# Optimization experiments

Measured on AMD Instinct MI355X. Metric: run time of the kernel, lower is better.

## Reference

```python
import jax, jax.numpy as jnp
import numpy as np

B, S, H, NH = 2, 2048, 1024, 16
HD = H // NH  # 64


def setup_inputs() -> dict:
    key = jax.random.key(0)
    ks = jax.random.split(key, 9)
    w = lambda k: jax.random.normal(k, (H, H), dtype=jnp.float32) * 0.02  # torch Linear weight [out,in]
    b = lambda k: jax.random.normal(k, (H,), dtype=jnp.float32) * 0.02
    return {
        "hidden_states": jax.random.normal(ks[0], (B, S, H), dtype=jnp.float32),
        "Wq": w(ks[1]), "bq": b(ks[2]),
        "Wk": w(ks[3]), "bk": b(ks[4]),
        "Wv": w(ks[5]), "bv": b(ks[6]),
        "Wo": w(ks[7]), "bo": b(ks[8]),
    }


def reference(hidden_states, Wq, bq, Wk, bk, Wv, bv, Wo, bo):
    b, s, h = hidden_states.shape
    nh, hd = NH, h // NH

    def proj(W, bias):
        y = hidden_states @ W.T + bias  # torch Linear: x W^T + b
        return y.reshape(b, s, nh, hd).transpose(0, 2, 1, 3)  # [b, h, s, d]

    q = proj(Wq, bq)
    k = proj(Wk, bk)
    v = proj(Wv, bv)

    scale = jnp.sqrt(jnp.asarray(hd, dtype=q.dtype))
    scores = jnp.einsum("bhqd,bhkd->bhqk", q, k) / scale  # [b, h, s, s]
    pos = jnp.arange(s)
    causal = pos[:, None] < pos[None, :]  # True where masked (key after query)
    scores = jnp.where(causal[None, None], -jnp.inf, scores)
    attn = jax.nn.softmax(scores, axis=-1)
    out = jnp.einsum("bhqk,bhkd->bhqd", attn, v)
    out = out.transpose(0, 2, 1, 3).reshape(b, s, h)
    return out @ Wo.T + bo
```

## Files before the change

kernel.cpp:

```cpp
#include <hip/hip_runtime.h>
#include <stdint.h>

typedef __bf16 bf16;
typedef __attribute__((ext_vector_type(2))) __bf16 bf16x2;
typedef __attribute__((ext_vector_type(4))) __bf16 bf16x4;
typedef __attribute__((ext_vector_type(8))) __bf16 bf16x8;
typedef __attribute__((ext_vector_type(4))) float f32x4;
typedef __attribute__((ext_vector_type(4))) short s16x4;

#define B_  2
#define S_  2048
#define H_  1024
#define NH_ 16
#define HD_ 64
#define RS  3072

__device__ __forceinline__ void glds16(const bf16* g, bf16* l) {
  __builtin_amdgcn_global_load_lds(
      (const __attribute__((address_space(1))) uint32_t*)g,
      (__attribute__((address_space(3))) uint32_t*)l, 16, 0, 0);
}

__device__ __forceinline__ f32x4 pv_mfma(bf16x4 a, bf16x4 b, f32x4 c) {
#if __has_builtin(__builtin_amdgcn_mfma_f32_16x16x16bf16_1k)
  union U { bf16x4 h; s16x4 s; };
  U ua; ua.h = a;
  U ub; ub.h = b;
  return __builtin_amdgcn_mfma_f32_16x16x16bf16_1k(ua.s, ub.s, c, 0, 0, 0);
#else
  f32x4 d;
  asm volatile("v_mfma_f32_16x16x16_bf16 %0, %1, %2, %3\n\ts_nop 7\n\ts_nop 7"
               : "=v"(d) : "v"(a), "v"(b), "v"(c));
  return d;
#endif
}

__global__ __launch_bounds__(256) void cvt_f32_bf16(
    const float* __restrict__ s0, bf16* __restrict__ d0, int n0,
    const float* __restrict__ s1, bf16* __restrict__ d1,
    const float* __restrict__ s2, bf16* __restrict__ d2,
    const float* __restrict__ s3, bf16* __restrict__ d3,
    const float* __restrict__ s4, bf16* __restrict__ d4, int nw)
{
  const float* s; bf16* d; int n;
  switch (blockIdx.y) {
    case 0:  s = s0; d = d0; n = n0; break;
    case 1:  s = s1; d = d1; n = nw; break;
    case 2:  s = s2; d = d2; n = nw; break;
    case 3:  s = s3; d = d3; n = nw; break;
    default: s = s4; d = d4; n = nw; break;
  }
  const int i = (blockIdx.x * 256 + threadIdx.x) * 8;
  if (i >= n) return;
  float4 v0 = *(const float4*)(s + i);
  float4 v1 = *(const float4*)(s + i + 4);
  bf16x8 o;
  o[0] = (bf16)v0.x; o[1] = (bf16)v0.y; o[2] = (bf16)v0.z; o[3] = (bf16)v0.w;
  o[4] = (bf16)v1.x; o[5] = (bf16)v1.y; o[6] = (bf16)v1.z; o[7] = (bf16)v1.w;
  *(bf16x8*)(d + i) = o;
}

__global__ __launch_bounds__(512, 2) void gemm_qkv_8ph(
    const bf16* __restrict__ X,
    const bf16* __restrict__ Wc,
    const float* __restrict__ bq, const float* __restrict__ bk,
    const float* __restrict__ bv,
    bf16* __restrict__ Y,
    float qscl)
{
  constexpr int K  = 1024;
  constexpr int NT = K / 64;

  __shared__ __align__(16) bf16 As[2][256 * 64];
  __shared__ __align__(16) bf16 Bs[2][256 * 64];

  const int f   = blockIdx.x;
  const int swz = (f & 7) * 24 + (f >> 3);
  const int by  = swz / 12, bx = swz % 12;
  const int m0  = by * 256, n0 = bx * 256;

  const int tid  = threadIdx.x;
  const int lane = tid & 63;
  const int wave = tid >> 6;
  const int quad = lane >> 4;
  const int l15  = lane & 15;
  const int wm   = (wave >> 2) * 128;
  const int wn   = (wave & 3) * 64;

  const int r0  = tid >> 3;
  const int kc0 = tid & 7;

  const bf16* Xb = X  + (size_t)m0 * K;
  const bf16* Wb = Wc + (size_t)n0 * K;

  f32x4 acc[8][4] = {};

#define SBAR() asm volatile("s_barrier" ::: "memory")
#define VM0()  asm volatile("s_waitcnt vmcnt(0)" ::: "memory")
#define STG(MAT, G, cb_, h)                                                 \
  { _Pragma("unroll") for (int s = 0; s < 2; ++s) {                         \
      const int row = (h) * 128 + s * 64 + r0;                              \
      const int sc  = kc0 ^ (row & 7);                                      \
      glds16((G) + (size_t)row * K + sc * 8,                                \
             &MAT[cb_][((h) * 1024 + s * 512 + wave * 64) * 8]); } }
#define RA(mi, ks) (*(const bf16x8*)&As[cb][(wm + (mi) * 16 + l15) * 64 +   \
                     ((((ks) * 4 + quad)) ^ (l15 & 7)) * 8])
#define RB(ni, ks) (*(const bf16x8*)&Bs[cb][(wn + (ni) * 16 + l15) * 64 +   \
                     ((((ks) * 4 + quad)) ^ (l15 & 7)) * 8])
#define MFMA(d, x, y) d = __builtin_amdgcn_mfma_f32_16x16x32_bf16(x, y, d, 0, 0, 0)

  STG(As, Xb, 0, 0); STG(As, Xb, 0, 1);
  STG(Bs, Wb, 0, 0); STG(Bs, Wb, 0, 1);
  VM0();
  SBAR();

  for (int t = 0; t < NT; ++t) {
    const int cb = t & 1, sb = cb ^ 1;
    const bf16* Xn = Xb + (t + 1) * 64;
    const bf16* Wn = Wb + (t + 1) * 64;
    const bool pre = (t + 1 < NT);

    bf16x8 a[4][2], b[4][2];

#pragma unroll
    for (int mi = 0; mi < 4; ++mi) { a[mi][0] = RA(mi, 0); a[mi][1] = RA(mi, 1); }
#pragma unroll
    for (int ni = 0; ni < 2; ++ni) { b[ni][0] = RB(ni, 0); b[ni][1] = RB(ni, 1); }
    if (pre) { STG(As, Xn, sb, 0); STG(As, Xn, sb, 1); }
    SBAR();
    __builtin_amdgcn_s_setprio(1);
#pragma unroll
    for (int mi = 0; mi < 4; ++mi)
#pragma unroll
      for (int ni = 0; ni < 2; ++ni) {
        MFMA(acc[mi][ni], a[mi][0], b[ni][0]);
        MFMA(acc[mi][ni], a[mi][1], b[ni][1]);
      }
    __builtin_amdgcn_s_setprio(0);
    SBAR();

#pragma unroll
    for (int ni = 2; ni < 4; ++ni) { b[ni][0] = RB(ni, 0); b[ni][1] = RB(ni, 1); }
    if (pre) { STG(Bs, Wn, sb, 0); STG(Bs, Wn, sb, 1); }
    SBAR();
    __builtin_amdgcn_s_setprio(1);
#pragma unroll
    for (int mi = 0; mi < 4; ++mi)
#pragma unroll
      for (int ni = 2; ni < 4; ++ni) {
        MFMA(acc[mi][ni], a[mi][0], b[ni][0]);
        MFMA(acc[mi][ni], a[mi][1], b[ni][1]);
      }
    __builtin_amdgcn_s_setprio(0);
    SBAR();

#pragma unroll
    for (int mi = 0; mi < 4; ++mi) { a[mi][0] = RA(mi + 4, 0); a[mi][1] = RA(mi + 4, 1); }
    SBAR();
    __builtin_amdgcn_s_setprio(1);
#pragma unroll
    for (int mi = 0; mi < 4; ++mi)
#pragma unroll
      for (int ni = 0; ni < 2; ++ni) {
        MFMA(acc[mi + 4][ni], a[mi][0], b[ni][0]);
        MFMA(acc[mi + 4][ni], a[mi][1], b[ni][1]);
      }
    __builtin_amdgcn_s_setprio(0);
    SBAR();

    __builtin_amdgcn_s_setprio(1);
#pragma unroll
    for (int mi = 0; mi < 4; ++mi)
#pragma unroll
      for (int ni = 2; ni < 4; ++ni) {
        MFMA(acc[mi + 4][ni], a[mi][0], b[ni][0]);
        MFMA(acc[mi + 4][ni], a[mi][1], b[ni][1]);
      }
    __builtin_amdgcn_s_setprio(0);
    VM0();
    SBAR();
  }

  const int seg = bx >> 2;
  const float* bias = seg == 0 ? bq : (seg == 1 ? bk : bv);
  const float ysc = seg == 0 ? qscl : 1.0f;
#pragma unroll
  for (int mi = 0; mi < 8; ++mi) {
    const int row = m0 + wm + mi * 16 + quad * 4;
#pragma unroll
    for (int ni = 0; ni < 4; ++ni) {
      const int col = n0 + wn + ni * 16 + l15;
      const float bvv = bias[col & 1023];
#pragma unroll
      for (int r = 0; r < 4; ++r)
        Y[(size_t)(row + r) * RS + col] = (bf16)((acc[mi][ni][r] + bvv) * ysc);
    }
  }
#undef SBAR
#undef VM0
#undef STG
#undef RA
#undef RB
#undef MFMA
}

template <typename TY>
__global__ __launch_bounds__(256) void gemm_bt_bias(
    const bf16* __restrict__ X,
    const bf16* __restrict__ W0, const bf16* __restrict__ W1, const bf16* __restrict__ W2,
    const float* __restrict__ b0, const float* __restrict__ b1, const float* __restrict__ b2,
    TY* __restrict__ Y0, TY* __restrict__ Y1, TY* __restrict__ Y2,
    float ys0, float ys1, float ys2,
    int M, int N, int K)
{
  const bf16* W; const float* bias; TY* Y; float ysc;
  if (blockIdx.z == 0)      { W = W0; bias = b0; Y = Y0; ysc = ys0; }
  else if (blockIdx.z == 1) { W = W1; bias = b1; Y = Y1; ysc = ys1; }
  else                      { W = W2; bias = b2; Y = Y2; ysc = ys2; }

  __shared__ __align__(16) bf16 As[2][128 * 32];
  __shared__ __align__(16) bf16 Bs[2][128 * 32];

  const int tid  = threadIdx.x;
  const int lane = tid & 63;
  const int wave = tid >> 6;
  const int m0 = blockIdx.y * 128;
  const int n0 = blockIdx.x * 128;
  const int wm = (wave >> 1) * 64;
  const int wn = (wave & 1) * 64;

  const int r0 = tid >> 2,            c0 = (tid & 3) * 8;
  const int r1 = (256 + tid) >> 2,    c1 = ((256 + tid) & 3) * 8;
  const int cb0 = (wave * 64) * 8;
  const int cb1 = (256 + wave * 64) * 8;

  f32x4 acc[4][4] = {};

  glds16(X + (size_t)(m0 + r0) * K + c0, &As[0][cb0]);
  glds16(W + (size_t)(n0 + r0) * K + c0, &Bs[0][cb0]);
  glds16(X + (size_t)(m0 + r1) * K + c1, &As[0][cb1]);
  glds16(W + (size_t)(n0 + r1) * K + c1, &Bs[0][cb1]);

  int pb = 0;
  for (int k0 = 0; k0 < K; k0 += 32, pb ^= 1) {
    __syncthreads();

    if (k0 + 32 < K) {
      const int kn = k0 + 32;
      glds16(X + (size_t)(m0 + r0) * K + kn + c0, &As[pb ^ 1][cb0]);
      glds16(W + (size_t)(n0 + r0) * K + kn + c0, &Bs[pb ^ 1][cb0]);
      glds16(X + (size_t)(m0 + r1) * K + kn + c1, &As[pb ^ 1][cb1]);
      glds16(W + (size_t)(n0 + r1) * K + kn + c1, &Bs[pb ^ 1][cb1]);
    }

    bf16x8 a[4], b[4];
#pragma unroll
    for (int i = 0; i < 4; ++i)
      a[i] = *(const bf16x8*)&As[pb][(wm + i * 16 + (lane & 15)) * 32 + (lane >> 4) * 8];
#pragma unroll
    for (int i = 0; i < 4; ++i)
      b[i] = *(const bf16x8*)&Bs[pb][(wn + i * 16 + (lane & 15)) * 32 + (lane >> 4) * 8];
#pragma unroll
    for (int mi = 0; mi < 4; ++mi)
#pragma unroll
      for (int ni = 0; ni < 4; ++ni)
        acc[mi][ni] = __builtin_amdgcn_mfma_f32_16x16x32_bf16(a[mi], b[ni], acc[mi][ni], 0, 0, 0);
  }

#pragma unroll
  for (int mi = 0; mi < 4; ++mi) {
    const int row = m0 + wm + mi * 16 + (lane >> 4) * 4;
#pragma unroll
    for (int ni = 0; ni < 4; ++ni) {
      const int col = n0 + wn + ni * 16 + (lane & 15);
      const float bv = bias[col];
#pragma unroll
      for (int r = 0; r < 4; ++r)
        Y[(size_t)(row + r) * N + col] = (TY)((acc[mi][ni][r] + bv) * ysc);
    }
  }
}

__device__ __forceinline__ void attn_tile_step(
    const bf16* Ksb, const bf16* Vtb, const bf16x8 bq[2], int qrow, int k0,
    bool maskit, float& mr, float& lr, f32x4 oacc[4], int l15, int quad)
{
  f32x4 sacc[8] = {};
  __builtin_amdgcn_s_setprio(1);
#pragma unroll
  for (int ks = 0; ks < 2; ++ks) {
#pragma unroll
    for (int mb = 0; mb < 8; ++mb) {
      const int row = mb * 16 + l15;
      const int ch  = (ks * 4 + quad) ^ (l15 & 7);
      bf16x8 ak = *(const bf16x8*)&Ksb[row * 64 + ch * 8];
      sacc[mb] = __builtin_amdgcn_mfma_f32_16x16x32_bf16(ak, bq[ks], sacc[mb], 0, 0, 0);
    }
  }
  __builtin_amdgcn_s_setprio(0);

  if (maskit) {
#pragma unroll
    for (int mb = 0; mb < 8; ++mb) {
      const int kb = k0 + mb * 16 + quad * 4;
#pragma unroll
      for (int r = 0; r < 4; ++r)
        if (kb + r > qrow) sacc[mb][r] = -1e30f;
    }
  }

  float mx = -1e30f;
#pragma unroll
  for (int mb = 0; mb < 8; ++mb)
    mx = fmaxf(mx, fmaxf(fmaxf(sacc[mb][0], sacc[mb][1]),
                         fmaxf(sacc[mb][2], sacc[mb][3])));
  mx = fmaxf(mx, __shfl_xor(mx, 16, 64));
  mx = fmaxf(mx, __shfl_xor(mx, 32, 64));

  float sum = 0.0f;
  bf16x4 pwv[8];
#pragma unroll
  for (int mb = 0; mb < 8; ++mb) {
    bf16x4 pw;
#pragma unroll
    for (int r = 0; r < 4; ++r) {
      const float p = __builtin_amdgcn_exp2f(sacc[mb][r] - mr);
      sum += p;
      pw[r] = (bf16)p;
    }
    pwv[mb] = pw;
  }
  sum += __shfl_xor(sum, 16, 64);
  sum += __shfl_xor(sum, 32, 64);

  __builtin_amdgcn_s_setprio(1);
#pragma unroll
  for (int mb = 0; mb < 8; ++mb) {
#pragma unroll
    for (int db = 0; db < 4; ++db) {
      const int vch = ((mb * 4 + quad) ^ (l15 & 7)) * 4;
      bf16x4 av = *(const bf16x4*)&Vtb[(db * 16 + l15) * 128 + vch];
      oacc[db] = pv_mfma(av, pwv[mb], oacc[db]);
    }
  }
  __builtin_amdgcn_s_setprio(0);

  lr += sum;
  if (!__all(mx <= mr + 8.0f)) {
    const float mnew  = fmaxf(mr, mx);
    const float alpha = __builtin_amdgcn_exp2f(mr - mnew);
    lr *= alpha;
#pragma unroll
    for (int db = 0; db < 4; ++db)
#pragma unroll
      for (int r = 0; r < 4; ++r) oacc[db][r] *= alpha;
    mr = mnew;
  }
}

__global__ __launch_bounds__(256, 2) void attn_causal(
    const bf16* __restrict__ QKV,
    bf16* __restrict__ O)
{
  const int lin  = blockIdx.x;
  const int slot = lin >> 3;
  const int bh   = (lin & 7) * 4 + (slot >> 4);
  const int pair = slot & 15;
  const int b    = bh >> 4;
  const int h    = bh & 15;

  const int tid  = threadIdx.x;
  const int lane = tid & 63;
  const int wave = tid >> 6;
  const int quad = lane >> 4;
  const int l15  = lane & 15;
  const size_t headq = (size_t)b * S_ * RS + (size_t)h * HD_;
  const size_t heado = (size_t)b * S_ * H_ + (size_t)h * HD_;
  const bf16* Qp = QKV + headq;
  const bf16* Kp = QKV + headq + 1024;
  const bf16* Vp = QKV + headq + 2048;

  __shared__ __align__(16) bf16 Ks[2][128 * 64];
  __shared__ __align__(16) bf16 Vt[2][64 * 128];

  const int qlo = pair, qhi = 31 - pair;
  const int nl  = (qlo >> 1) + 1;
  const int nh  = (qhi >> 1) + 1;
  const int qrowL = qlo * 64 + wave * 16 + l15;
  const int qrowH = qhi * 64 + wave * 16 + l15;

  bf16x8 bqL[2], bqH[2];
  bqL[0] = *(const bf16x8*)(Qp + (size_t)qrowL * RS + quad * 8);
  bqL[1] = *(const bf16x8*)(Qp + (size_t)qrowL * RS + 32 + quad * 8);
  bqH[0] = *(const bf16x8*)(Qp + (size_t)qrowH * RS + quad * 8);
  bqH[1] = *(const bf16x8*)(Qp + (size_t)qrowH * RS + 32 + quad * 8);

  const int vr = lane * 2;
  const int vc = wave * 16;

#define STAGE_K(k0_, buf_)                                                  \
  {                                                                         \
    _Pragma("unroll")                                                       \
    for (int i = 0; i < 4; ++i) {                                           \
      const int n = i * 256 + tid;                                          \
      const int row = n >> 3;                                               \
      const int cg  = (n & 7) ^ (row & 7);                                  \
      glds16(Kp + (size_t)((k0_) + row) * RS + cg * 8,                      \
             &Ks[buf_][(i * 256 + wave * 64) * 8]);                         \
    }                                                                       \
  }

#define LOAD_V(k0_)                                                         \
  {                                                                         \
    vreg[0] = *(const bf16x8*)(Vp + (size_t)((k0_) + vr) * RS + vc);        \
    vreg[1] = *(const bf16x8*)(Vp + (size_t)((k0_) + vr) * RS + vc + 8);    \
    vreg[2] = *(const bf16x8*)(Vp + (size_t)((k0_) + vr + 1) * RS + vc);    \
    vreg[3] = *(const bf16x8*)(Vp + (size_t)((k0_) + vr + 1) * RS + vc + 8);\
  }

#define WRITE_V(buf_)                                                       \
  {                                                                         \
    _Pragma("unroll")                                                       \
    for (int e = 0; e < 8; ++e) {                                           \
      const int sw = (((vr >> 2) ^ e) * 4) + (vr & 3);                      \
      bf16x2 p0; p0[0] = vreg[0][e]; p0[1] = vreg[2][e];                    \
      *(bf16x2*)&Vt[buf_][(vc + e) * 128 + sw] = p0;                        \
      bf16x2 p1; p1[0] = vreg[1][e]; p1[1] = vreg[3][e];                    \
      *(bf16x2*)&Vt[buf_][(vc + 8 + e) * 128 + sw] = p1;                    \
    }                                                                       \
  }

  bf16x8 vreg[4];

  STAGE_K(0, 0);
  LOAD_V(0);
  WRITE_V(0);
  __syncthreads();

  float mrL = 0.0f, lrL = 0.0f, mrH = 0.0f, lrH = 0.0f;
  f32x4 oL[4] = {}, oH[4] = {};

  for (int it = 0; it < nh; ++it) {
    const int c = it & 1;
    const bool pre = (it + 1 < nh);

    if (pre) {
      STAGE_K((it + 1) * 128, c ^ 1);
      LOAD_V((it + 1) * 128);
    }

    attn_tile_step(Ks[c], Vt[c], bqH, qrowH, it * 128, it == nh - 1,
                   mrH, lrH, oH, l15, quad);
    if (it < nl)
      attn_tile_step(Ks[c], Vt[c], bqL, qrowL, it * 128, it == nl - 1,
                     mrL, lrL, oL, l15, quad);

    if (pre) {
      WRITE_V(c ^ 1);
      __syncthreads();
    }
  }

  const float invL = 1.0f / lrL;
#pragma unroll
  for (int db = 0; db < 4; ++db) {
    bf16x4 o;
#pragma unroll
    for (int r = 0; r < 4; ++r) o[r] = (bf16)(oL[db][r] * invL);
    *(bf16x4*)(O + heado + (size_t)qrowL * H_ + db * 16 + quad * 4) = o;
  }
  const float invH = 1.0f / lrH;
#pragma unroll
  for (int db = 0; db < 4; ++db) {
    bf16x4 o;
#pragma unroll
    for (int r = 0; r < 4; ++r) o[r] = (bf16)(oH[db][r] * invH);
    *(bf16x4*)(O + heado + (size_t)qrowH * H_ + db * 16 + quad * 4) = o;
  }
#undef STAGE_K
#undef LOAD_V
#undef WRITE_V
}

extern "C" void kernel_launch(void* const* d_in, const int* in_sizes, int n_in,
                              void* d_out, int out_size, void* d_ws, size_t ws_size,
                              hipStream_t stream) {
  const float* hs = (const float*)d_in[0];
  const float* Wq = (const float*)d_in[1]; const float* bq = (const float*)d_in[2];
  const float* Wk = (const float*)d_in[3]; const float* bk = (const float*)d_in[4];
  const float* Wv = (const float*)d_in[5]; const float* bv = (const float*)d_in[6];
  const float* Wo = (const float*)d_in[7]; const float* bo = (const float*)d_in[8];
  float* out = (float*)d_out;

  const size_t elems = (size_t)B_ * S_ * H_;
  const size_t wel   = (size_t)H_ * H_;
  bf16* hsb  = (bf16*)d_ws;
  bf16* AO   = hsb;
  bf16* Wqb  = hsb + elems;
  bf16* Wkb  = Wqb + wel;
  bf16* Wvb  = Wkb + wel;
  bf16* Wob  = Wvb + wel;
  bf16* Ycat = Wob + wel;

  cvt_f32_bf16<<<dim3(2048, 5), dim3(256), 0, stream>>>(
      hs, hsb, (int)elems, Wq, Wqb, Wk, Wkb, Wv, Wvb, Wo, Wob, (int)wel);

  const int M = B_ * S_;
  const float QSCL = 0.125f * 1.44269504f;

  gemm_qkv_8ph<<<dim3(192), dim3(512), 0, stream>>>(
      hsb, Wqb, bq, bk, bv, Ycat, QSCL);

  attn_causal<<<dim3(512), dim3(256), 0, stream>>>(Ycat, AO);

  gemm_bt_bias<float><<<dim3(H_ / 128, M / 128, 1), dim3(256), 0, stream>>>(
      AO, Wob, Wob, Wob, bo, bo, bo, out, out, out, 1.0f, 1.0f, 1.0f, M, H_, H_);
}
```

Before: 200.7 us.

## Split attention blocks into 8 waves with separate Q/K/V buffers

The attention kernel now runs 512 threads per block. Four waves handle the high query tile and four handle the low one, where before each wave processed both tiles in sequence. This raises parallelism and shortens the per-wave critical path, but waves on the low tile sit idle through the later iterations. The QKV GEMM now writes separate Q, K and V buffers with row stride 1024 instead of one interleaved 3072-stride buffer. The V transpose staging and its LDS swizzle are reworked, and the output GEMM signature is simplified.

```diff
diff --git a/kernel.cpp b/kernel.cpp
--- a/kernel.cpp
+++ b/kernel.cpp
@@ -13,7 +13,6 @@
 #define H_  1024
 #define NH_ 16
 #define HD_ 64
-#define RS  3072
 
 __device__ __forceinline__ void glds16(const bf16* g, bf16* l) {
   __builtin_amdgcn_global_load_lds(
@@ -65,7 +64,7 @@
     const bf16* __restrict__ Wc,
     const float* __restrict__ bq, const float* __restrict__ bk,
     const float* __restrict__ bv,
-    bf16* __restrict__ Y,
+    bf16* __restrict__ Yq, bf16* __restrict__ Yk, bf16* __restrict__ Yv,
     float qscl)
 {
   constexpr int K  = 1024;
@@ -183,17 +182,19 @@
 
   const int seg = bx >> 2;
   const float* bias = seg == 0 ? bq : (seg == 1 ? bk : bv);
+  bf16* Yp = seg == 0 ? Yq : (seg == 1 ? Yk : Yv);
   const float ysc = seg == 0 ? qscl : 1.0f;
+  const int nc0 = n0 - seg * 1024;
 #pragma unroll
   for (int mi = 0; mi < 8; ++mi) {
     const int row = m0 + wm + mi * 16 + quad * 4;
 #pragma unroll
     for (int ni = 0; ni < 4; ++ni) {
-      const int col = n0 + wn + ni * 16 + l15;
-      const float bvv = bias[col & 1023];
+      const int col = nc0 + wn + ni * 16 + l15;
+      const float bvv = bias[col];
 #pragma unroll
       for (int r = 0; r < 4; ++r)
-        Y[(size_t)(row + r) * RS + col] = (bf16)((acc[mi][ni][r] + bvv) * ysc);
+        Yp[(size_t)(row + r) * H_ + col] = (bf16)((acc[mi][ni][r] + bvv) * ysc);
     }
   }
 #undef SBAR
@@ -206,18 +207,10 @@
 
 template <typename TY>
 __global__ __launch_bounds__(256) void gemm_bt_bias(
-    const bf16* __restrict__ X,
-    const bf16* __restrict__ W0, const bf16* __restrict__ W1, const bf16* __restrict__ W2,
-    const float* __restrict__ b0, const float* __restrict__ b1, const float* __restrict__ b2,
-    TY* __restrict__ Y0, TY* __restrict__ Y1, TY* __restrict__ Y2,
-    float ys0, float ys1, float ys2,
+    const bf16* __restrict__ X, const bf16* __restrict__ W,
+    const float* __restrict__ bias, TY* __restrict__ Y,
     int M, int N, int K)
 {
-  const bf16* W; const float* bias; TY* Y; float ysc;
-  if (blockIdx.z == 0)      { W = W0; bias = b0; Y = Y0; ysc = ys0; }
-  else if (blockIdx.z == 1) { W = W1; bias = b1; Y = Y1; ysc = ys1; }
-  else                      { W = W2; bias = b2; Y = Y2; ysc = ys2; }
-
   __shared__ __align__(16) bf16 As[2][128 * 32];
   __shared__ __align__(16) bf16 Bs[2][128 * 32];
 
@@ -276,7 +269,7 @@
       const float bv = bias[col];
 #pragma unroll
       for (int r = 0; r < 4; ++r)
-        Y[(size_t)(row + r) * N + col] = (TY)((acc[mi][ni][r] + bv) * ysc);
+        Y[(size_t)(row + r) * N + col] = (TY)(acc[mi][ni][r] + bv);
     }
   }
 }
@@ -338,8 +331,8 @@
   for (int mb = 0; mb < 8; ++mb) {
 #pragma unroll
     for (int db = 0; db < 4; ++db) {
-      const int vch = ((mb * 4 + quad) ^ (l15 & 7)) * 4;
-      bf16x4 av = *(const bf16x4*)&Vtb[(db * 16 + l15) * 128 + vch];
+      const int vch = (mb * 4 + quad) ^ ((l15 & 7) << 2) ^ ((l15 >> 3) & 1) ^ (db << 1);
+      bf16x4 av = *(const bf16x4*)&Vtb[(db * 16 + l15) * 128 + vch * 4];
       oacc[db] = pv_mfma(av, pwv[mb], oacc[db]);
     }
   }
@@ -358,9 +351,9 @@
   }
 }
 
-__global__ __launch_bounds__(256, 2) void attn_causal(
-    const bf16* __restrict__ QKV,
-    bf16* __restrict__ O)
+__global__ __launch_bounds__(512, 4) void attn_causal(
+    const bf16* __restrict__ Q, const bf16* __restrict__ K,
+    const bf16* __restrict__ V, bf16* __restrict__ O)
 {
   const int lin  = blockIdx.x;
   const int slot = lin >> 3;
@@ -374,11 +367,9 @@
   const int wave = tid >> 6;
   const int quad = lane >> 4;
   const int l15  = lane & 15;
-  const size_t headq = (size_t)b * S_ * RS + (size_t)h * HD_;
-  const size_t heado = (size_t)b * S_ * H_ + (size_t)h * HD_;
-  const bf16* Qp = QKV + headq;
-  const bf16* Kp = QKV + headq + 1024;
-  const bf16* Vp = QKV + headq + 2048;
+  const size_t headoff = (size_t)b * S_ * H_ + (size_t)h * HD_;
+  const bf16* Kp = K + headoff;
+  const bf16* Vp = V + headoff;
 
   __shared__ __align__(16) bf16 Ks[2][128 * 64];
   __shared__ __align__(16) bf16 Vt[2][64 * 128];
@@ -386,59 +377,57 @@
   const int qlo = pair, qhi = 31 - pair;
   const int nl  = (qlo >> 1) + 1;
   const int nh  = (qhi >> 1) + 1;
-  const int qrowL = qlo * 64 + wave * 16 + l15;
-  const int qrowH = qhi * 64 + wave * 16 + l15;
-
-  bf16x8 bqL[2], bqH[2];
-  bqL[0] = *(const bf16x8*)(Qp + (size_t)qrowL * RS + quad * 8);
-  bqL[1] = *(const bf16x8*)(Qp + (size_t)qrowL * RS + 32 + quad * 8);
-  bqH[0] = *(const bf16x8*)(Qp + (size_t)qrowH * RS + quad * 8);
-  bqH[1] = *(const bf16x8*)(Qp + (size_t)qrowH * RS + 32 + quad * 8);
-
-  const int vr = lane * 2;
-  const int vc = wave * 16;
+  const bool isH = wave < 4;
+  const int  myq = isH ? qhi : qlo;
+  const int  myn = isH ? nh  : nl;
+  const int qrow = myq * 64 + (wave & 3) * 16 + l15;
+
+  bf16x8 bq[2];
+  bq[0] = *(const bf16x8*)(Q + headoff + (size_t)qrow * H_ + quad * 8);
+  bq[1] = *(const bf16x8*)(Q + headoff + (size_t)qrow * H_ + 32 + quad * 8);
+
+  const int kp = tid & 63;
+  const int g  = tid >> 6;
 
 #define STAGE_K(k0_, buf_)                                                  \
   {                                                                         \
     _Pragma("unroll")                                                       \
-    for (int i = 0; i < 4; ++i) {                                           \
-      const int n = i * 256 + tid;                                          \
+    for (int i = 0; i < 2; ++i) {                                           \
+      const int n = i * 512 + tid;                                          \
       const int row = n >> 3;                                               \
       const int cg  = (n & 7) ^ (row & 7);                                  \
-      glds16(Kp + (size_t)((k0_) + row) * RS + cg * 8,                      \
-             &Ks[buf_][(i * 256 + wave * 64) * 8]);                         \
+      glds16(Kp + (size_t)((k0_) + row) * H_ + cg * 8,                      \
+             &Ks[buf_][(i * 512 + wave * 64) * 8]);                         \
     }                                                                       \
   }
 
 #define LOAD_V(k0_)                                                         \
   {                                                                         \
-    vreg[0] = *(const bf16x8*)(Vp + (size_t)((k0_) + vr) * RS + vc);        \
-    vreg[1] = *(const bf16x8*)(Vp + (size_t)((k0_) + vr) * RS + vc + 8);    \
-    vreg[2] = *(const bf16x8*)(Vp + (size_t)((k0_) + vr + 1) * RS + vc);    \
-    vreg[3] = *(const bf16x8*)(Vp + (size_t)((k0_) + vr + 1) * RS + vc + 8);\
+    vreg[0] = *(const bf16x8*)(Vp + (size_t)((k0_) + 2 * kp) * H_ + g * 8); \
+    vreg[1] = *(const bf16x8*)(Vp + (size_t)((k0_) + 2 * kp + 1) * H_ + g * 8);\
   }
 
 #define WRITE_V(buf_)                                                       \
   {                                                                         \
     _Pragma("unroll")                                                       \
     for (int e = 0; e < 8; ++e) {                                           \
-      const int sw = (((vr >> 2) ^ e) * 4) + (vr & 3);                      \
-      bf16x2 p0; p0[0] = vreg[0][e]; p0[1] = vreg[2][e];                    \
-      *(bf16x2*)&Vt[buf_][(vc + e) * 128 + sw] = p0;                        \
-      bf16x2 p1; p1[0] = vreg[1][e]; p1[1] = vreg[3][e];                    \
-      *(bf16x2*)&Vt[buf_][(vc + 8 + e) * 128 + sw] = p1;                    \
+      const int row = g * 8 + e;                                            \
+      const int pos = (kp >> 1) ^ ((row & 7) << 2) ^ ((row >> 3) & 1)       \
+                      ^ ((row >> 4) << 1);                                  \
+      bf16x2 pw; pw[0] = vreg[0][e]; pw[1] = vreg[1][e];                    \
+      *(bf16x2*)&Vt[buf_][row * 128 + pos * 4 + ((2 * kp) & 3)] = pw;       \
     }                                                                       \
   }
 
-  bf16x8 vreg[4];
+  bf16x8 vreg[2];
 
   STAGE_K(0, 0);
   LOAD_V(0);
   WRITE_V(0);
   __syncthreads();
 
-  float mrL = 0.0f, lrL = 0.0f, mrH = 0.0f, lrH = 0.0f;
-  f32x4 oL[4] = {}, oH[4] = {};
+  float mr = 0.0f, lr = 0.0f;
+  f32x4 oacc[4] = {};
 
   for (int it = 0; it < nh; ++it) {
     const int c = it & 1;
@@ -449,11 +438,9 @@
       LOAD_V((it + 1) * 128);
     }
 
-    attn_tile_step(Ks[c], Vt[c], bqH, qrowH, it * 128, it == nh - 1,
-                   mrH, lrH, oH, l15, quad);
-    if (it < nl)
-      attn_tile_step(Ks[c], Vt[c], bqL, qrowL, it * 128, it == nl - 1,
-                     mrL, lrL, oL, l15, quad);
+    if (it < myn)
+      attn_tile_step(Ks[c], Vt[c], bq, qrow, it * 128, it == myn - 1,
+                     mr, lr, oacc, l15, quad);
 
     if (pre) {
       WRITE_V(c ^ 1);
@@ -461,21 +448,13 @@
     }
   }
 
-  const float invL = 1.0f / lrL;
+  const float inv = 1.0f / lr;
 #pragma unroll
   for (int db = 0; db < 4; ++db) {
     bf16x4 o;
 #pragma unroll
-    for (int r = 0; r < 4; ++r) o[r] = (bf16)(oL[db][r] * invL);
-    *(bf16x4*)(O + heado + (size_t)qrowL * H_ + db * 16 + quad * 4) = o;
-  }
-  const float invH = 1.0f / lrH;
-#pragma unroll
-  for (int db = 0; db < 4; ++db) {
-    bf16x4 o;
-#pragma unroll
-    for (int r = 0; r < 4; ++r) o[r] = (bf16)(oH[db][r] * invH);
-    *(bf16x4*)(O + heado + (size_t)qrowH * H_ + db * 16 + quad * 4) = o;
+    for (int r = 0; r < 4; ++r) o[r] = (bf16)(oacc[db][r] * inv);
+    *(bf16x4*)(O + headoff + (size_t)qrow * H_ + db * 16 + quad * 4) = o;
   }
 #undef STAGE_K
 #undef LOAD_V
@@ -494,13 +473,15 @@
 
   const size_t elems = (size_t)B_ * S_ * H_;
   const size_t wel   = (size_t)H_ * H_;
-  bf16* hsb  = (bf16*)d_ws;
-  bf16* AO   = hsb;
-  bf16* Wqb  = hsb + elems;
-  bf16* Wkb  = Wqb + wel;
-  bf16* Wvb  = Wkb + wel;
-  bf16* Wob  = Wvb + wel;
-  bf16* Ycat = Wob + wel;
+  bf16* hsb = (bf16*)d_ws;
+  bf16* AO  = hsb;
+  bf16* Wqb = hsb + elems;
+  bf16* Wkb = Wqb + wel;
+  bf16* Wvb = Wkb + wel;
+  bf16* Wob = Wvb + wel;
+  bf16* Qw  = Wob + wel;
+  bf16* Kw  = Qw + elems;
+  bf16* Vw  = Kw + elems;
 
   cvt_f32_bf16<<<dim3(2048, 5), dim3(256), 0, stream>>>(
       hs, hsb, (int)elems, Wq, Wqb, Wk, Wkb, Wv, Wvb, Wo, Wob, (int)wel);
@@ -509,10 +490,10 @@
   const float QSCL = 0.125f * 1.44269504f;
 
   gemm_qkv_8ph<<<dim3(192), dim3(512), 0, stream>>>(
-      hsb, Wqb, bq, bk, bv, Ycat, QSCL);
-
-  attn_causal<<<dim3(512), dim3(256), 0, stream>>>(Ycat, AO);
-
-  gemm_bt_bias<float><<<dim3(H_ / 128, M / 128, 1), dim3(256), 0, stream>>>(
-      AO, Wob, Wob, Wob, bo, bo, bo, out, out, out, 1.0f, 1.0f, 1.0f, M, H_, H_);
-}
+      hsb, Wqb, bq, bk, bv, Qw, Kw, Vw, QSCL);
+
+  attn_causal<<<dim3(512), dim3(512), 0, stream>>>(Qw, Kw, Vw, AO);
+
+  gemm_bt_bias<float><<<dim3(H_ / 128, M / 128), dim3(256), 0, stream>>>(
+      AO, Wob, bo, out, M, H_, H_);
+}
```

Result: no change. 204.5 us (+1.9%).
